# Optimization experiments

Hardware: AMD Instinct MI355X
Metric: run time of the kernel (lower is better)

The kernel has to match this reference:

```python
import jax, jax.numpy as jnp
import numpy as np
import math

B, T, D, H, K = 4, 2048, 1024, 16, 64

def setup_inputs() -> dict:
    key = jax.random.key(0)
    ks = jax.random.split(key, 6)
    scale = 1.0 / math.sqrt(D)  # keep logits in a sane range (torch code uses raw randn params)
    X = jax.random.normal(ks[0], (B, T, D), dtype=jnp.float32)
    Wq = jax.random.normal(ks[1], (H, D, K), dtype=jnp.float32) * scale
    Wk = jax.random.normal(ks[2], (H, D, K), dtype=jnp.float32) * scale
    Wv = jax.random.normal(ks[3], (H, D, K), dtype=jnp.float32) * scale
    Wo = jax.random.normal(ks[4], (H * K, H * K), dtype=jnp.float32) * (1.0 / math.sqrt(H * K))
    bo = jnp.zeros((H * K,), dtype=jnp.float32)
    return {"X": X, "Wq": Wq, "Wk": Wk, "Wv": Wv, "Wo": Wo, "bo": bo}

def reference(X, Wq, Wk, Wv, Wo, bo):
    # per-head projections: [B,H,T,K]
    q = jnp.einsum('btc,nck->bntk', X, Wq)
    k = jnp.einsum('btc,nck->bntk', X, Wk)
    v = jnp.einsum('btc,nck->bntk', X, Wv)
    # full score matrix [B,H,T,T] with causal mask (query t attends to s <= t)
    scores = jnp.einsum('bntk,bnsk->bnts', q, k) / math.sqrt(K)
    causal = jnp.tril(jnp.ones((T, T), dtype=bool))
    scores = jnp.where(causal[None, None], scores, jnp.finfo(scores.dtype).min)
    attn = jax.nn.softmax(scores, axis=-1)
    out = jnp.einsum('bnts,bnsk->bntk', attn, v)  # [B,H,T,K]
    # concat heads along feature dim (head-major ordering, matches torch.cat over heads)
    out = jnp.transpose(out, (0, 2, 1, 3)).reshape(B, T, H * K)
    # output projection (torch nn.Linear: x @ W.T + b)
    return out @ Wo.T + bo
```

## Files before the change

### kernel.cpp

```cpp
#include <hip/hip_runtime.h>
#include <hip/hip_bf16.h>
#include <math.h>

#define B_SZ 4
#define T_SZ 2048
#define D_SZ 1024
#define H_SZ 16
#define K_SZ 64

typedef __attribute__((ext_vector_type(8))) short bf8_t;
typedef __attribute__((ext_vector_type(4))) float f4_t;

__device__ __forceinline__ ushort f2bf(float f) {
    union { float f; unsigned u; } v; v.f = f;
    return (ushort)((v.u + 0x7fffu + ((v.u >> 16) & 1u)) >> 16);
}

__device__ __forceinline__ uint cvt_pk_bf16(float lo, float hi) {
    uint r;
    asm("v_cvt_pk_bf16_f32 %0, %1, %2" : "=v"(r) : "v"(lo), "v"(hi));
    return r;
}

__device__ __forceinline__ void gld_lds16(const ushort* g, ushort* l) {
    __builtin_amdgcn_global_load_lds(
        (const __attribute__((address_space(1))) void*)g,
        (__attribute__((address_space(3))) void*)l, 16, 0, 0);
}

#define Q_PRESCALE 0.18033688011112042f

__global__ __launch_bounds__(256) void convert_bf16_kernel(
    const float* __restrict__ src, ushort* __restrict__ dst)
{
    const size_t i = ((size_t)blockIdx.x * 256 + threadIdx.x) * 8;
    float4 a = *(const float4*)(src + i);
    float4 b = *(const float4*)(src + i + 4);
    ushort o[8] = {f2bf(a.x), f2bf(a.y), f2bf(a.z), f2bf(a.w),
                   f2bf(b.x), f2bf(b.y), f2bf(b.z), f2bf(b.w)};
    *(uint4*)(dst + i) = *(const uint4*)o;
}

__global__ __launch_bounds__(256) void transpose_w_kernel(
    const float* __restrict__ Wq, const float* __restrict__ Wk,
    const float* __restrict__ Wv, ushort* __restrict__ WT)
{
    __shared__ __align__(16) float tile[64][68];
    const int tid = threadIdx.x;
    const int d0  = blockIdx.x * 64;
    const int g   = blockIdx.y;
    const int sel = g >> 4, h = g & 15;
    const float* W = (sel == 0 ? Wq : (sel == 1 ? Wk : Wv)) + (size_t)h * D_SZ * K_SZ;

    {
        const int r = tid >> 2, ks = (tid & 3) * 16;
        const float4* src = (const float4*)(W + (size_t)(d0 + r) * 64 + ks);
        float4* dst = (float4*)&tile[r][ks];
        dst[0] = src[0]; dst[1] = src[1]; dst[2] = src[2]; dst[3] = src[3];
    }
    __syncthreads();
    {
        const int k = tid >> 2, ds = (tid & 3) * 16;
        ushort o[16];
        #pragma unroll
        for (int i = 0; i < 16; ++i) o[i] = f2bf(tile[ds + i][k]);
        uint4* dst = (uint4*)&WT[(size_t)(sel * 1024 + h * 64 + k) * 1024 + d0 + ds];
        dst[0] = ((const uint4*)o)[0];
        dst[1] = ((const uint4*)o)[1];
    }
}

__device__ __forceinline__ void gemm_bt_tile(
    const ushort* __restrict__ A, const ushort* __restrict__ Bt,
    int Kdim, int m0, int n0, ushort* As, ushort* Bs, f4_t acc[4][4])
{
    const int tid  = threadIdx.x;
    const int lane = tid & 63, wv = tid >> 6;
    const int l16  = lane & 15, quad = lane >> 4;
    const int wm   = (wv >> 1) * 64, wn = (wv & 1) * 64;
    const int sw   = (l16 >> 1) & 3;

    const int ra0 = tid >> 2,         qa0 = (tid & 3) ^ ((ra0 >> 1) & 3);
    const int ra1 = (tid + 256) >> 2, qa1 = (tid & 3) ^ ((ra1 >> 1) & 3);
    ushort* ldsA0 = As + (size_t)(wv * 64) * 8;
    ushort* ldsA1 = As + (size_t)(wv * 64 + 256) * 8;
    ushort* ldsB0 = Bs + (size_t)(wv * 64) * 8;
    ushort* ldsB1 = Bs + (size_t)(wv * 64 + 256) * 8;
    const ushort* gA0 = A  + (size_t)(m0 + ra0) * Kdim + qa0 * 8;
    const ushort* gA1 = A  + (size_t)(m0 + ra1) * Kdim + qa1 * 8;
    const ushort* gB0 = Bt + (size_t)(n0 + ra0) * Kdim + qa0 * 8;
    const ushort* gB1 = Bt + (size_t)(n0 + ra1) * Kdim + qa1 * 8;

    for (int k0 = 0; k0 < Kdim; k0 += 32) {
        __syncthreads();
        gld_lds16(gA0 + k0, ldsA0);
        gld_lds16(gA1 + k0, ldsA1);
        gld_lds16(gB0 + k0, ldsB0);
        gld_lds16(gB1 + k0, ldsB1);
        __syncthreads();

        bf8_t a[4], b[4];
        #pragma unroll
        for (int mt = 0; mt < 4; ++mt)
            a[mt] = *(const bf8_t*)&As[(wm + mt * 16 + l16) * 32 + ((quad ^ sw) * 8)];
        #pragma unroll
        for (int nt = 0; nt < 4; ++nt)
            b[nt] = *(const bf8_t*)&Bs[(wn + nt * 16 + l16) * 32 + ((quad ^ sw) * 8)];
        #pragma unroll
        for (int mt = 0; mt < 4; ++mt)
            #pragma unroll
            for (int nt = 0; nt < 4; ++nt)
                acc[mt][nt] = __builtin_amdgcn_mfma_f32_16x16x32_bf16(
                    a[mt], b[nt], acc[mt][nt], 0, 0, 0);
    }
}

__global__ __launch_bounds__(256) void gemm_qkv_kernel(
    const ushort* __restrict__ Xb, const ushort* __restrict__ WT,
    ushort* __restrict__ Qo, ushort* __restrict__ Ko, ushort* __restrict__ Vo)
{
    __shared__ __align__(16) ushort As[128 * 32];
    __shared__ __align__(16) ushort Bs[128 * 32];
    const int n0 = blockIdx.x * 128, m0 = blockIdx.y * 128;

    f4_t acc[4][4];
    #pragma unroll
    for (int i = 0; i < 4; ++i)
        #pragma unroll
        for (int j = 0; j < 4; ++j) acc[i][j] = (f4_t){0.f, 0.f, 0.f, 0.f};

    gemm_bt_tile(Xb, WT, 1024, m0, n0, As, Bs, acc);

    const int tid = threadIdx.x;
    const int lane = tid & 63, wv = tid >> 6;
    const int l16 = lane & 15, quad = lane >> 4;
    const int wm = (wv >> 1) * 64, wn = (wv & 1) * 64;
    const int sel = n0 >> 10;
    ushort* Out = (sel == 0 ? Qo : (sel == 1 ? Ko : Vo));
    const float osc = (sel == 0) ? Q_PRESCALE : 1.0f;

    #pragma unroll
    for (int nt = 0; nt < 4; ++nt) {
        const int col = n0 + wn + nt * 16 + l16;
        const int h = (col >> 6) & 15, kk = col & 63;
        #pragma unroll
        for (int mt = 0; mt < 4; ++mt) {
            #pragma unroll
            for (int r = 0; r < 4; ++r) {
                const int row = m0 + wm + mt * 16 + quad * 4 + r;
                const int bb = row >> 11, t = row & 2047;
                Out[((size_t)(bb * 16 + h) * 2048 + t) * 64 + kk] =
                    f2bf(acc[mt][nt][r] * osc);
            }
        }
    }
}

__global__ __launch_bounds__(256) void gemm_out_kernel(
    const ushort* __restrict__ Yb, const ushort* __restrict__ WoB,
    const float* __restrict__ bo, float* __restrict__ Out)
{
    __shared__ __align__(16) ushort As[128 * 32];
    __shared__ __align__(16) ushort Bs[128 * 32];
    const int n0 = blockIdx.x * 128, m0 = blockIdx.y * 128;

    f4_t acc[4][4];
    #pragma unroll
    for (int i = 0; i < 4; ++i)
        #pragma unroll
        for (int j = 0; j < 4; ++j) acc[i][j] = (f4_t){0.f, 0.f, 0.f, 0.f};

    gemm_bt_tile(Yb, WoB, 1024, m0, n0, As, Bs, acc);

    const int tid = threadIdx.x;
    const int lane = tid & 63, wv = tid >> 6;
    const int l16 = lane & 15, quad = lane >> 4;
    const int wm = (wv >> 1) * 64, wn = (wv & 1) * 64;

    #pragma unroll
    for (int nt = 0; nt < 4; ++nt) {
        const int col = n0 + wn + nt * 16 + l16;
        const float bias = bo[col];
        #pragma unroll
        for (int mt = 0; mt < 4; ++mt) {
            #pragma unroll
            for (int r = 0; r < 4; ++r) {
                const int row = m0 + wm + mt * 16 + quad * 4 + r;
                Out[(size_t)row * 1024 + col] = acc[mt][nt][r] + bias;
            }
        }
    }
}

__global__ __launch_bounds__(256) void transpose_v_kernel(
    const ushort* __restrict__ V, ushort* __restrict__ Vt)
{
    __shared__ __align__(16) ushort tile[64 * 74];
    const int tid = threadIdx.x;
    const int t0  = blockIdx.x * 64;
    const int bh  = blockIdx.y;

    {
        const int t = tid >> 2, ks = (tid & 3) * 16;
        const ushort* src = V + ((size_t)bh * T_SZ + t0 + t) * K_SZ + ks;
        uint4 a = *(const uint4*)src;
        uint4 b = *(const uint4*)(src + 8);
        uint* dst = (uint*)&tile[t * 74 + ks];
        dst[0] = a.x; dst[1] = a.y; dst[2] = a.z; dst[3] = a.w;
        dst[4] = b.x; dst[5] = b.y; dst[6] = b.z; dst[7] = b.w;
    }
    __syncthreads();
    {
        const int l = tid & 63, w = tid >> 6;
        #pragma unroll
        for (int kk = 0; kk < 16; ++kk) {
            const int k = w * 16 + kk;
            Vt[((size_t)bh * K_SZ + k) * T_SZ + t0 + l] = tile[l * 74 + k];
        }
    }
}

__global__ __launch_bounds__(64, 2) void attn_mfma_kernel(
    const ushort* __restrict__ Qg, const ushort* __restrict__ Kg,
    const ushort* __restrict__ Vtg, ushort* __restrict__ Y)
{
    __shared__ __align__(16) ushort Ph[2][32 * 72];

    const int lane = threadIdx.x;
    const int l16  = lane & 15;
    const int quad = lane >> 4;

    const int lin = blockIdx.x;
    const int xcd = lin & 7;
    const int idx = lin >> 3;
    const int bh  = xcd * 8 + (idx & 7);
    const int jp  = idx >> 3;
    const int bb  = bh >> 4, h = bh & 15;

    const int trowL = jp * 32;
    const int trowH = (63 - jp) * 32;

    const ushort* Kbh = Kg  + (size_t)bh * T_SZ * K_SZ;
    const ushort* Vbh = Vtg + (size_t)bh * K_SZ * T_SZ;

    bf8_t qaL[2][2], qaH[2][2];
    #pragma unroll
    for (int mt = 0; mt < 2; ++mt) {
        const ushort* qpL = Qg + ((size_t)bh * T_SZ + trowL + mt * 16 + l16) * K_SZ + quad * 8;
        const ushort* qpH = Qg + ((size_t)bh * T_SZ + trowH + mt * 16 + l16) * K_SZ + quad * 8;
        qaL[mt][0] = *(const bf8_t*)qpL;
        qaL[mt][1] = *(const bf8_t*)(qpL + 32);
        qaH[mt][0] = *(const bf8_t*)qpH;
        qaH[mt][1] = *(const bf8_t*)(qpH + 32);
    }

    f4_t OL[2][4], OH[2][4];
    float lpL[2] = {0.f, 0.f}, lpH[2] = {0.f, 0.f};
    #pragma unroll
    for (int mt = 0; mt < 2; ++mt)
        #pragma unroll
        for (int dt = 0; dt < 4; ++dt) {
            OL[mt][dt] = (f4_t){0.f, 0.f, 0.f, 0.f};
            OH[mt][dt] = (f4_t){0.f, 0.f, 0.f, 0.f};
        }

    const int n_it = (trowH + 32 + 63) >> 6;

    bf8_t kb[4][2], vb[4][2];
    #pragma unroll
    for (int nt = 0; nt < 4; ++nt)
        #pragma unroll
        for (int hh = 0; hh < 2; ++hh) {
            kb[nt][hh] = *(const bf8_t*)&Kbh[(size_t)(nt * 16 + l16) * K_SZ + hh * 32 + quad * 8];
            vb[nt][hh] = *(const bf8_t*)&Vbh[(size_t)(nt * 16 + l16) * T_SZ + hh * 32 + quad * 8];
        }

    auto qk = [&](const bf8_t (&qa)[2][2], f4_t (&S)[4][2]) {
        #pragma unroll
        for (int nt = 0; nt < 4; ++nt)
            #pragma unroll
            for (int mt = 0; mt < 2; ++mt) {
                S[nt][mt] = (f4_t){0.f, 0.f, 0.f, 0.f};
                S[nt][mt] = __builtin_amdgcn_mfma_f32_16x16x32_bf16(
                    kb[nt][0], qa[mt][0], S[nt][mt], 0, 0, 0);
                S[nt][mt] = __builtin_amdgcn_mfma_f32_16x16x32_bf16(
                    kb[nt][1], qa[mt][1], S[nt][mt], 0, 0, 0);
            }
    };

    auto sm_pv = [&](f4_t (&S)[4][2], f4_t (&O)[2][4], float (&lp)[2],
                     int trow, ushort* myP, int s0) {
        const bool diag = (s0 + 64 > trow);

        #pragma unroll
        for (int mt = 0; mt < 2; ++mt) {
            const int qg = trow + mt * 16 + l16;
            #pragma unroll
            for (int nt = 0; nt < 4; ++nt) {
                float p[4];
                if (diag) {
                    #pragma unroll
                    for (int r = 0; r < 4; ++r) {
                        float x = S[nt][mt][r];
                        if (s0 + nt * 16 + quad * 4 + r > qg) x = -1e30f;
                        p[r] = __builtin_amdgcn_exp2f(x);
                    }
                } else {
                    #pragma unroll
                    for (int r = 0; r < 4; ++r)
                        p[r] = __builtin_amdgcn_exp2f(S[nt][mt][r]);
                }
                lp[mt] += (p[0] + p[1]) + (p[2] + p[3]);
                uint2 pk;
                pk.x = cvt_pk_bf16(p[0], p[1]);
                pk.y = cvt_pk_bf16(p[2], p[3]);
                *(uint2*)&myP[(mt * 16 + l16) * 72 + nt * 16 + quad * 4] = pk;
            }
        }
        asm volatile("" ::: "memory");
        bf8_t pa[2][2];
        #pragma unroll
        for (int mt = 0; mt < 2; ++mt) {
            const ushort* pr = &myP[(mt * 16 + l16) * 72];
            pa[mt][0] = *(const bf8_t*)(pr + quad * 8);
            pa[mt][1] = *(const bf8_t*)(pr + 32 + quad * 8);
        }
        asm volatile("" ::: "memory");

        #pragma unroll
        for (int dt = 0; dt < 4; ++dt)
            #pragma unroll
            for (int mt = 0; mt < 2; ++mt) {
                O[mt][dt] = __builtin_amdgcn_mfma_f32_16x16x32_bf16(
                    pa[mt][0], vb[dt][0], O[mt][dt], 0, 0, 0);
                O[mt][dt] = __builtin_amdgcn_mfma_f32_16x16x32_bf16(
                    pa[mt][1], vb[dt][1], O[mt][dt], 0, 0, 0);
            }
    };

    for (int it = 0; it < n_it; ++it) {
        const int s0 = it * 64;
        const bool doL  = (s0 < trowL + 32);
        const bool more = (it + 1 < n_it);
        const int  sn   = s0 + 64;

        f4_t S[4][2];

        qk(qaH, S);
        sm_pv(S, OH, lpH, trowH, Ph[0], s0);

        if (doL) qk(qaL, S);

        if (more) {
            #pragma unroll
            for (int nt = 0; nt < 4; ++nt)
                #pragma unroll
                for (int hh = 0; hh < 2; ++hh)
                    kb[nt][hh] = *(const bf8_t*)&Kbh[
                        (size_t)(sn + nt * 16 + l16) * K_SZ + hh * 32 + quad * 8];
        }

        if (doL) sm_pv(S, OL, lpL, trowL, Ph[1], s0);

        if (more) {
            #pragma unroll
            for (int nt = 0; nt < 4; ++nt)
                #pragma unroll
                for (int hh = 0; hh < 2; ++hh)
                    vb[nt][hh] = *(const bf8_t*)&Vbh[
                        (size_t)(nt * 16 + l16) * T_SZ + sn + hh * 32 + quad * 8];
        }
    }

    auto epilogue = [&](f4_t (&O)[2][4], float (&lp)[2], int trow) {
        #pragma unroll
        for (int mt = 0; mt < 2; ++mt) {
            float s = lp[mt];
            s += __shfl_xor(s, 16);
            s += __shfl_xor(s, 32);
            const float inv = 1.f / s;
            float invr[4];
            #pragma unroll
            for (int r = 0; r < 4; ++r)
                invr[r] = __shfl(inv, quad * 4 + r);
            #pragma unroll
            for (int dt = 0; dt < 4; ++dt) {
                const int col = h * 64 + dt * 16 + l16;
                #pragma unroll
                for (int r = 0; r < 4; ++r) {
                    const int tg = trow + mt * 16 + quad * 4 + r;
                    Y[((size_t)(bb * T_SZ + tg)) * (H_SZ * K_SZ) + col] =
                        f2bf(O[mt][dt][r] * invr[r]);
                }
            }
        }
    };
    epilogue(OH, lpH, trowH);
    epilogue(OL, lpL, trowL);
}

extern "C" void kernel_launch(void* const* d_in, const int* in_sizes, int n_in,
                              void* d_out, int out_size, void* d_ws, size_t ws_size,
                              hipStream_t stream) {
    const float* X  = (const float*)d_in[0];
    const float* Wq = (const float*)d_in[1];
    const float* Wk = (const float*)d_in[2];
    const float* Wv = (const float*)d_in[3];
    const float* Wo = (const float*)d_in[4];
    const float* bo = (const float*)d_in[5];
    float* out = (float*)d_out;

    const size_t NE = (size_t)B_SZ * H_SZ * T_SZ * K_SZ;
    ushort* Qb   = (ushort*)d_ws;
    ushort* Kb   = Qb + NE;
    ushort* Vb   = Kb + NE;
    ushort* Vtb  = Vb + NE;
    ushort* Yb   = Vtb + NE;
    ushort* Xb   = Yb + NE;
    ushort* WT   = Xb + NE;
    ushort* WoB  = WT + (size_t)3072 * 1024;

    convert_bf16_kernel<<<dim3(4096), 256, 0, stream>>>(X, Xb);
    convert_bf16_kernel<<<dim3(512), 256, 0, stream>>>(Wo, WoB);
    transpose_w_kernel<<<dim3(16, 48), 256, 0, stream>>>(Wq, Wk, Wv, WT);
    gemm_qkv_kernel<<<dim3(24, 64), 256, 0, stream>>>(Xb, WT, Qb, Kb, Vb);
    transpose_v_kernel<<<dim3(32, 64), 256, 0, stream>>>(Vb, Vtb);
    attn_mfma_kernel<<<dim3(2048), 64, 0, stream>>>(Qb, Kb, Vtb, Yb);
    gemm_out_kernel<<<dim3(8, 64), 256, 0, stream>>>(Yb, WoB, bo, out);
}
```

Before: 297.6 us.

## Split paired causal query tiles into separate single-wave blocks

Each attention block previously processed a low and a high 32-row query tile together, sharing each K/V fetch across both. Now each block handles one tile, the grid is doubled, and launch bounds allow 4 waves per SIMD with halved LDS. This is meant to cut per-wave register pressure and raise occupancy and latency hiding. In exchange, K/V tiles are reloaded separately for each query tile, and per-block work is now unbalanced, so the scheduler must even out the load.

Result: slower. 641.1 us (+115.4%).

```diff
diff --git a/kernel.cpp b/kernel.cpp
--- a/kernel.cpp
+++ b/kernel.cpp
@@ -220,11 +220,11 @@
     }
 }
 
-__global__ __launch_bounds__(64, 2) void attn_mfma_kernel(
+__global__ __launch_bounds__(64, 4) void attn_mfma_kernel(
     const ushort* __restrict__ Qg, const ushort* __restrict__ Kg,
     const ushort* __restrict__ Vtg, ushort* __restrict__ Y)
 {
-    __shared__ __align__(16) ushort Ph[2][32 * 72];
+    __shared__ __align__(16) ushort Ph[32 * 72];
 
     const int lane = threadIdx.x;
     const int l16  = lane & 15;
@@ -234,37 +234,32 @@
     const int xcd = lin & 7;
     const int idx = lin >> 3;
     const int bh  = xcd * 8 + (idx & 7);
-    const int jp  = idx >> 3;
+    const int rem = idx >> 3;
+    const int jp  = rem >> 1;
+    const int j   = (rem & 1) ? (63 - jp) : jp;
     const int bb  = bh >> 4, h = bh & 15;
 
-    const int trowL = jp * 32;
-    const int trowH = (63 - jp) * 32;
+    const int trow = j * 32;
 
     const ushort* Kbh = Kg  + (size_t)bh * T_SZ * K_SZ;
     const ushort* Vbh = Vtg + (size_t)bh * K_SZ * T_SZ;
 
-    bf8_t qaL[2][2], qaH[2][2];
+    bf8_t qa[2][2];
     #pragma unroll
     for (int mt = 0; mt < 2; ++mt) {
-        const ushort* qpL = Qg + ((size_t)bh * T_SZ + trowL + mt * 16 + l16) * K_SZ + quad * 8;
-        const ushort* qpH = Qg + ((size_t)bh * T_SZ + trowH + mt * 16 + l16) * K_SZ + quad * 8;
-        qaL[mt][0] = *(const bf8_t*)qpL;
-        qaL[mt][1] = *(const bf8_t*)(qpL + 32);
-        qaH[mt][0] = *(const bf8_t*)qpH;
-        qaH[mt][1] = *(const bf8_t*)(qpH + 32);
-    }
-
-    f4_t OL[2][4], OH[2][4];
-    float lpL[2] = {0.f, 0.f}, lpH[2] = {0.f, 0.f};
+        const ushort* qp = Qg + ((size_t)bh * T_SZ + trow + mt * 16 + l16) * K_SZ + quad * 8;
+        qa[mt][0] = *(const bf8_t*)qp;
+        qa[mt][1] = *(const bf8_t*)(qp + 32);
+    }
+
+    f4_t O[2][4];
+    float lp[2] = {0.f, 0.f};
     #pragma unroll
     for (int mt = 0; mt < 2; ++mt)
         #pragma unroll
-        for (int dt = 0; dt < 4; ++dt) {
-            OL[mt][dt] = (f4_t){0.f, 0.f, 0.f, 0.f};
-            OH[mt][dt] = (f4_t){0.f, 0.f, 0.f, 0.f};
-        }
-
-    const int n_it = (trowH + 32 + 63) >> 6;
+        for (int dt = 0; dt < 4; ++dt) O[mt][dt] = (f4_t){0.f, 0.f, 0.f, 0.f};
+
+    const int n_it = (trow + 32 + 63) >> 6;
 
     bf8_t kb[4][2], vb[4][2];
     #pragma unroll
@@ -275,7 +270,12 @@
             vb[nt][hh] = *(const bf8_t*)&Vbh[(size_t)(nt * 16 + l16) * T_SZ + hh * 32 + quad * 8];
         }
 
-    auto qk = [&](const bf8_t (&qa)[2][2], f4_t (&S)[4][2]) {
+    for (int it = 0; it < n_it; ++it) {
+        const int s0 = it * 64;
+        const bool more = (it + 1 < n_it);
+        const int  sn   = s0 + 64;
+
+        f4_t S[4][2];
         #pragma unroll
         for (int nt = 0; nt < 4; ++nt)
             #pragma unroll
@@ -286,12 +286,17 @@
                 S[nt][mt] = __builtin_amdgcn_mfma_f32_16x16x32_bf16(
                     kb[nt][1], qa[mt][1], S[nt][mt], 0, 0, 0);
             }
-    };
-
-    auto sm_pv = [&](f4_t (&S)[4][2], f4_t (&O)[2][4], float (&lp)[2],
-                     int trow, ushort* myP, int s0) {
+
+        if (more) {
+            #pragma unroll
+            for (int nt = 0; nt < 4; ++nt)
+                #pragma unroll
+                for (int hh = 0; hh < 2; ++hh)
+                    kb[nt][hh] = *(const bf8_t*)&Kbh[
+                        (size_t)(sn + nt * 16 + l16) * K_SZ + hh * 32 + quad * 8];
+        }
+
         const bool diag = (s0 + 64 > trow);
-
         #pragma unroll
         for (int mt = 0; mt < 2; ++mt) {
             const int qg = trow + mt * 16 + l16;
@@ -314,14 +319,14 @@
                 uint2 pk;
                 pk.x = cvt_pk_bf16(p[0], p[1]);
                 pk.y = cvt_pk_bf16(p[2], p[3]);
-                *(uint2*)&myP[(mt * 16 + l16) * 72 + nt * 16 + quad * 4] = pk;
+                *(uint2*)&Ph[(mt * 16 + l16) * 72 + nt * 16 + quad * 4] = pk;
             }
         }
         asm volatile("" ::: "memory");
         bf8_t pa[2][2];
         #pragma unroll
         for (int mt = 0; mt < 2; ++mt) {
-            const ushort* pr = &myP[(mt * 16 + l16) * 72];
+            const ushort* pr = &Ph[(mt * 16 + l16) * 72];
             pa[mt][0] = *(const bf8_t*)(pr + quad * 8);
             pa[mt][1] = *(const bf8_t*)(pr + 32 + quad * 8);
         }
@@ -336,31 +341,6 @@
                 O[mt][dt] = __builtin_amdgcn_mfma_f32_16x16x32_bf16(
                     pa[mt][1], vb[dt][1], O[mt][dt], 0, 0, 0);
             }
-    };
-
-    for (int it = 0; it < n_it; ++it) {
-        const int s0 = it * 64;
-        const bool doL  = (s0 < trowL + 32);
-        const bool more = (it + 1 < n_it);
-        const int  sn   = s0 + 64;
-
-        f4_t S[4][2];
-
-        qk(qaH, S);
-        sm_pv(S, OH, lpH, trowH, Ph[0], s0);
-
-        if (doL) qk(qaL, S);
-
-        if (more) {
-            #pragma unroll
-            for (int nt = 0; nt < 4; ++nt)
-                #pragma unroll
-                for (int hh = 0; hh < 2; ++hh)
-                    kb[nt][hh] = *(const bf8_t*)&Kbh[
-                        (size_t)(sn + nt * 16 + l16) * K_SZ + hh * 32 + quad * 8];
-        }
-
-        if (doL) sm_pv(S, OL, lpL, trowL, Ph[1], s0);
 
         if (more) {
             #pragma unroll
@@ -372,31 +352,27 @@
         }
     }
 
-    auto epilogue = [&](f4_t (&O)[2][4], float (&lp)[2], int trow) {
-        #pragma unroll
-        for (int mt = 0; mt < 2; ++mt) {
-            float s = lp[mt];
-            s += __shfl_xor(s, 16);
-            s += __shfl_xor(s, 32);
-            const float inv = 1.f / s;
-            float invr[4];
-            #pragma unroll
-            for (int r = 0; r < 4; ++r)
-                invr[r] = __shfl(inv, quad * 4 + r);
-            #pragma unroll
-            for (int dt = 0; dt < 4; ++dt) {
-                const int col = h * 64 + dt * 16 + l16;
-                #pragma unroll
-                for (int r = 0; r < 4; ++r) {
-                    const int tg = trow + mt * 16 + quad * 4 + r;
-                    Y[((size_t)(bb * T_SZ + tg)) * (H_SZ * K_SZ) + col] =
-                        f2bf(O[mt][dt][r] * invr[r]);
-                }
-            }
-        }
-    };
-    epilogue(OH, lpH, trowH);
-    epilogue(OL, lpL, trowL);
+    #pragma unroll
+    for (int mt = 0; mt < 2; ++mt) {
+        float s = lp[mt];
+        s += __shfl_xor(s, 16);
+        s += __shfl_xor(s, 32);
+        const float inv = 1.f / s;
+        float invr[4];
+        #pragma unroll
+        for (int r = 0; r < 4; ++r)
+            invr[r] = __shfl(inv, quad * 4 + r);
+        #pragma unroll
+        for (int dt = 0; dt < 4; ++dt) {
+            const int col = h * 64 + dt * 16 + l16;
+            #pragma unroll
+            for (int r = 0; r < 4; ++r) {
+                const int tg = trow + mt * 16 + quad * 4 + r;
+                Y[((size_t)(bb * T_SZ + tg)) * (H_SZ * K_SZ) + col] =
+                    f2bf(O[mt][dt][r] * invr[r]);
+            }
+        }
+    }
 }
 
 extern "C" void kernel_launch(void* const* d_in, const int* in_sizes, int n_in,
@@ -425,6 +401,6 @@
     transpose_w_kernel<<<dim3(16, 48), 256, 0, stream>>>(Wq, Wk, Wv, WT);
     gemm_qkv_kernel<<<dim3(24, 64), 256, 0, stream>>>(Xb, WT, Qb, Kb, Vb);
     transpose_v_kernel<<<dim3(32, 64), 256, 0, stream>>>(Vb, Vtb);
-    attn_mfma_kernel<<<dim3(2048), 64, 0, stream>>>(Qb, Kb, Vtb, Yb);
+    attn_mfma_kernel<<<dim3(4096), 64, 0, stream>>>(Qb, Kb, Vtb, Yb);
     gemm_out_kernel<<<dim3(8, 64), 256, 0, stream>>>(Yb, WoB, bo, out);
 }
```

## Split attention KV range across two waves per block and merge partial sums

Applied to the files above, without the earlier changes.

The attention kernel now launches two wavefronts per block instead of one. Wave 0 processes the first half of the key/value range for both the high and low query tiles, and wave 1 processes the remaining key/value blocks. The partial O accumulators and row sums are exchanged through shared memory, after which each wave writes one tile. This raises per-block parallelism and shortens the serial KV loop, at the cost of extra LDS traffic and barriers. Dropping the min-blocks launch bound also changes register allocation.

Result: slower. 315.7 us (+6.1%).

```diff
diff --git a/kernel.cpp b/kernel.cpp
--- a/kernel.cpp
+++ b/kernel.cpp
@@ -220,13 +220,15 @@
     }
 }
 
-__global__ __launch_bounds__(64, 2) void attn_mfma_kernel(
+__global__ __launch_bounds__(128) void attn_mfma_kernel(
     const ushort* __restrict__ Qg, const ushort* __restrict__ Kg,
     const ushort* __restrict__ Vtg, ushort* __restrict__ Y)
 {
     __shared__ __align__(16) ushort Ph[2][32 * 72];
 
-    const int lane = threadIdx.x;
+    const int tid  = threadIdx.x;
+    const int w    = tid >> 6;
+    const int lane = tid & 63;
     const int l16  = lane & 15;
     const int quad = lane >> 4;
 
@@ -234,11 +236,15 @@
     const int xcd = lin & 7;
     const int idx = lin >> 3;
     const int bh  = xcd * 8 + (idx & 7);
-    const int jp  = idx >> 3;
+    const int p   = idx >> 3;
     const int bb  = bh >> 4, h = bh & 15;
 
-    const int trowL = jp * 32;
-    const int trowH = (63 - jp) * 32;
+    const int trowL = p * 32;
+    const int trowH = (63 - p) * 32;
+    const int T_L = (trowL + 32 + 63) >> 6;
+    const int T_H = (trowH + 32 + 63) >> 6;
+    const int hL  = (T_L + 1) >> 1;
+    const int hH  = (T_H + 1) >> 1;
 
     const ushort* Kbh = Kg  + (size_t)bh * T_SZ * K_SZ;
     const ushort* Vbh = Vtg + (size_t)bh * K_SZ * T_SZ;
@@ -264,16 +270,25 @@
             OH[mt][dt] = (f4_t){0.f, 0.f, 0.f, 0.f};
         }
 
-    const int n_it = (trowH + 32 + 63) >> 6;
+    ushort* myP = Ph[w];
 
     bf8_t kb[4][2], vb[4][2];
-    #pragma unroll
-    for (int nt = 0; nt < 4; ++nt)
-        #pragma unroll
-        for (int hh = 0; hh < 2; ++hh) {
-            kb[nt][hh] = *(const bf8_t*)&Kbh[(size_t)(nt * 16 + l16) * K_SZ + hh * 32 + quad * 8];
-            vb[nt][hh] = *(const bf8_t*)&Vbh[(size_t)(nt * 16 + l16) * T_SZ + hh * 32 + quad * 8];
-        }
+    auto loadK = [&](int s0) {
+        #pragma unroll
+        for (int nt = 0; nt < 4; ++nt)
+            #pragma unroll
+            for (int hh = 0; hh < 2; ++hh)
+                kb[nt][hh] = *(const bf8_t*)&Kbh[
+                    (size_t)(s0 + nt * 16 + l16) * K_SZ + hh * 32 + quad * 8];
+    };
+    auto loadV = [&](int s0) {
+        #pragma unroll
+        for (int nt = 0; nt < 4; ++nt)
+            #pragma unroll
+            for (int hh = 0; hh < 2; ++hh)
+                vb[nt][hh] = *(const bf8_t*)&Vbh[
+                    (size_t)(nt * 16 + l16) * T_SZ + s0 + hh * 32 + quad * 8];
+    };
 
     auto qk = [&](const bf8_t (&qa)[2][2], f4_t (&S)[4][2]) {
         #pragma unroll
@@ -287,33 +302,31 @@
                     kb[nt][1], qa[mt][1], S[nt][mt], 0, 0, 0);
             }
     };
-
     auto sm_pv = [&](f4_t (&S)[4][2], f4_t (&O)[2][4], float (&lp)[2],
-                     int trow, ushort* myP, int s0) {
+                     int trow, int s0) {
         const bool diag = (s0 + 64 > trow);
-
         #pragma unroll
         for (int mt = 0; mt < 2; ++mt) {
             const int qg = trow + mt * 16 + l16;
             #pragma unroll
             for (int nt = 0; nt < 4; ++nt) {
-                float p[4];
+                float pr[4];
                 if (diag) {
                     #pragma unroll
                     for (int r = 0; r < 4; ++r) {
                         float x = S[nt][mt][r];
                         if (s0 + nt * 16 + quad * 4 + r > qg) x = -1e30f;
-                        p[r] = __builtin_amdgcn_exp2f(x);
+                        pr[r] = __builtin_amdgcn_exp2f(x);
                     }
                 } else {
                     #pragma unroll
                     for (int r = 0; r < 4; ++r)
-                        p[r] = __builtin_amdgcn_exp2f(S[nt][mt][r]);
+                        pr[r] = __builtin_amdgcn_exp2f(S[nt][mt][r]);
                 }
-                lp[mt] += (p[0] + p[1]) + (p[2] + p[3]);
+                lp[mt] += (pr[0] + pr[1]) + (pr[2] + pr[3]);
                 uint2 pk;
-                pk.x = cvt_pk_bf16(p[0], p[1]);
-                pk.y = cvt_pk_bf16(p[2], p[3]);
+                pk.x = cvt_pk_bf16(pr[0], pr[1]);
+                pk.y = cvt_pk_bf16(pr[2], pr[3]);
                 *(uint2*)&myP[(mt * 16 + l16) * 72 + nt * 16 + quad * 4] = pk;
             }
         }
@@ -326,7 +339,6 @@
             pa[mt][1] = *(const bf8_t*)(pr + 32 + quad * 8);
         }
         asm volatile("" ::: "memory");
-
         #pragma unroll
         for (int dt = 0; dt < 4; ++dt)
             #pragma unroll
@@ -338,41 +350,90 @@
             }
     };
 
-    for (int it = 0; it < n_it; ++it) {
-        const int s0 = it * 64;
-        const bool doL  = (s0 < trowL + 32);
-        const bool more = (it + 1 < n_it);
-        const int  sn   = s0 + 64;
-
-        f4_t S[4][2];
-
-        qk(qaH, S);
-        sm_pv(S, OH, lpH, trowH, Ph[0], s0);
-
-        if (doL) qk(qaL, S);
-
-        if (more) {
-            #pragma unroll
-            for (int nt = 0; nt < 4; ++nt)
+    if (w == 0) {
+        loadK(0); loadV(0);
+        for (int it = 0; it < hH; ++it) {
+            const int s0 = it * 64;
+            const bool more = (it + 1 < hH);
+            const bool doL  = (it < hL);
+            f4_t S[4][2];
+            qk(qaH, S);
+            sm_pv(S, OH, lpH, trowH, s0);
+            if (doL) qk(qaL, S);
+            if (more) loadK(s0 + 64);
+            if (doL) sm_pv(S, OL, lpL, trowL, s0);
+            if (more) loadV(s0 + 64);
+        }
+    } else {
+        loadK(hH * 64); loadV(hH * 64);
+        for (int it = hH; it < T_H; ++it) {
+            const int s0 = it * 64;
+            const bool more = (it + 1 < T_H);
+            f4_t S[4][2];
+            qk(qaH, S);
+            if (more) loadK(s0 + 64);
+            sm_pv(S, OH, lpH, trowH, s0);
+            if (more) loadV(s0 + 64);
+        }
+        if (hL < T_L) {
+            loadK(hL * 64); loadV(hL * 64);
+            for (int it = hL; it < T_L; ++it) {
+                const int s0 = it * 64;
+                const bool more = (it + 1 < T_L);
+                f4_t S[4][2];
+                qk(qaL, S);
+                if (more) loadK(s0 + 64);
+                sm_pv(S, OL, lpL, trowL, s0);
+                if (more) loadV(s0 + 64);
+            }
+        }
+    }
+
+    float* M = (float*)&Ph[0][0];
+    const int mb = lane * 34;
+    __syncthreads();
+    if (w == 1) {
+        #pragma unroll
+        for (int mt = 0; mt < 2; ++mt)
+            #pragma unroll
+            for (int dt = 0; dt < 4; ++dt)
                 #pragma unroll
-                for (int hh = 0; hh < 2; ++hh)
-                    kb[nt][hh] = *(const bf8_t*)&Kbh[
-                        (size_t)(sn + nt * 16 + l16) * K_SZ + hh * 32 + quad * 8];
-        }
-
-        if (doL) sm_pv(S, OL, lpL, trowL, Ph[1], s0);
-
-        if (more) {
-            #pragma unroll
-            for (int nt = 0; nt < 4; ++nt)
+                for (int r = 0; r < 4; ++r)
+                    M[mb + mt * 16 + dt * 4 + r] = OH[mt][dt][r];
+        M[mb + 32] = lpH[0]; M[mb + 33] = lpH[1];
+    }
+    __syncthreads();
+    if (w == 0) {
+        #pragma unroll
+        for (int mt = 0; mt < 2; ++mt)
+            #pragma unroll
+            for (int dt = 0; dt < 4; ++dt)
                 #pragma unroll
-                for (int hh = 0; hh < 2; ++hh)
-                    vb[nt][hh] = *(const bf8_t*)&Vbh[
-                        (size_t)(nt * 16 + l16) * T_SZ + sn + hh * 32 + quad * 8];
-        }
-    }
-
-    auto epilogue = [&](f4_t (&O)[2][4], float (&lp)[2], int trow) {
+                for (int r = 0; r < 4; ++r)
+                    OH[mt][dt][r] += M[mb + mt * 16 + dt * 4 + r];
+        lpH[0] += M[mb + 32]; lpH[1] += M[mb + 33];
+        #pragma unroll
+        for (int mt = 0; mt < 2; ++mt)
+            #pragma unroll
+            for (int dt = 0; dt < 4; ++dt)
+                #pragma unroll
+                for (int r = 0; r < 4; ++r)
+                    M[mb + mt * 16 + dt * 4 + r] = OL[mt][dt][r];
+        M[mb + 32] = lpL[0]; M[mb + 33] = lpL[1];
+    }
+    __syncthreads();
+    if (w == 1) {
+        #pragma unroll
+        for (int mt = 0; mt < 2; ++mt)
+            #pragma unroll
+            for (int dt = 0; dt < 4; ++dt)
+                #pragma unroll
+                for (int r = 0; r < 4; ++r)
+                    OL[mt][dt][r] += M[mb + mt * 16 + dt * 4 + r];
+        lpL[0] += M[mb + 32]; lpL[1] += M[mb + 33];
+    }
+
+    auto epi = [&](f4_t (&O)[2][4], float (&lp)[2], int trow) {
         #pragma unroll
         for (int mt = 0; mt < 2; ++mt) {
             float s = lp[mt];
@@ -395,8 +456,8 @@
             }
         }
     };
-    epilogue(OH, lpH, trowH);
-    epilogue(OL, lpL, trowL);
+    if (w == 0) epi(OH, lpH, trowH);
+    else        epi(OL, lpL, trowL);
 }
 
 extern "C" void kernel_launch(void* const* d_in, const int* in_sizes, int n_in,
@@ -425,6 +486,6 @@
     transpose_w_kernel<<<dim3(16, 48), 256, 0, stream>>>(Wq, Wk, Wv, WT);
     gemm_qkv_kernel<<<dim3(24, 64), 256, 0, stream>>>(Xb, WT, Qb, Kb, Vb);
     transpose_v_kernel<<<dim3(32, 64), 256, 0, stream>>>(Vb, Vtb);
-    attn_mfma_kernel<<<dim3(2048), 64, 0, stream>>>(Qb, Kb, Vtb, Yb);
+    attn_mfma_kernel<<<dim3(2048), 128, 0, stream>>>(Qb, Kb, Vtb, Yb);
     gemm_out_kernel<<<dim3(8, 64), 256, 0, stream>>>(Yb, WoB, bo, out);
 }
```
